# Kernel tuning notes

Measured on AMD Instinct MI355X. Metric: run time of the kernel, lower is better.

The kernel has to match this reference:

```python
import jax, jax.numpy as jnp
import numpy as np

# Dims: B=2, T=4 -> BT=8 frames; S=H*W=256 tokens/frame; L=25 stacked LLM layers; D=4096 llm hidden
BT, S, L, D = 8, 256, 25, 4096
C, NH = 1024, 8          # teacher_hid_size (hard-coded), num_heads
HD = C // NH             # 128
LAYER_IDX = np.array([24, 20, 16, 12, 8, 4, 0])  # num_layer=24 - arange(0,25,4)
J = len(LAYER_IDX)       # 7 distillation layers
SCALE = C ** -0.5        # NOTE: teacher_hid_size**-0.5, NOT head_dim**-0.5 (faithful to source)
EPS_LN, EPS_COS = 1e-5, 1e-8


def setup_inputs() -> dict:
    key = jax.random.key(0)
    ks = jax.random.split(key, 7)
    def n(k, shape, s=1.0):
        return jax.random.normal(k, shape, dtype=jnp.float32) * s
    return {
        "all_features": n(ks[0], (BT, S, L, D)),
        "teacher_features": n(ks[1], (BT, S, C)),
        "ln_gamma": jnp.ones((J, D), jnp.float32),
        "ln_beta": jnp.zeros((J, D), jnp.float32),
        "norm_w": n(ks[2], (J, C, D), 0.02),   # per-layer Linear(llm->teacher), no bias
        "input_w": n(ks[3], (C, D), 0.02),
        "input_b": n(ks[4], (C,), 0.02),
        "output_w": n(ks[5], (C, C), 0.02),
        "output_b": n(ks[6], (C,), 0.02),
    }


def reference(all_features, teacher_features, ln_gamma, ln_beta, norm_w,
              input_w, input_b, output_w, output_b):
    # Gather the distilled layers: [BT, S, J, D]
    x = all_features[:, :, LAYER_IDX]
    # Per-layer LayerNorm (each norm_layer[j] has its own affine params)
    mu = x.mean(-1, keepdims=True)
    var = ((x - mu) ** 2).mean(-1, keepdims=True)
    xn = (x - mu) * jax.lax.rsqrt(var + EPS_LN) * ln_gamma + ln_beta
    # Per-layer Linear (bias=False): stack -> vision_outputs [BT, S, J, C]
    vo = jnp.einsum('bsjd,jcd->bsjc', xn, norm_w)
    # input_layer on last hidden state: vision_input [BT, S, C]
    vin = jnp.einsum('bsd,cd->bsc', all_features[:, :, -1], input_w) + input_b
    # Hand-rolled multiplicative cross-attention over the J layer axis
    voh = vo.reshape(BT, S, J, NH, HD)
    q = voh[:, :, 0]        # [BT, S, NH, HD]
    kv = voh[:, :, 1:]      # [BT, S, J-1, NH, HD]
    scores = jnp.einsum('bshd,bskhd->bshk', q * SCALE, kv)   # [BT, S, NH, J-1]
    attn = jax.nn.softmax(scores, axis=-1)
    fuse = jnp.einsum('bshk,bskhd->bshd', attn, kv).reshape(BT, S, C)
    vf = vin + jnp.einsum('bsc,oc->bso', fuse, output_w) + output_b  # vision_feature
    # Cosine distillation loss vs teacher (torch CosineSimilarity eps=1e-8)
    na = jnp.maximum(jnp.linalg.norm(vf, axis=-1), EPS_COS)
    nb = jnp.maximum(jnp.linalg.norm(teacher_features, axis=-1), EPS_COS)
    cos = (vf * teacher_features).sum(-1) / (na * nb)        # [BT, S]
    # sum_i (1 - mean_s cos_i) / count_image, count_image = BT  ->  1 - mean over all
    return 1.0 - cos.mean()
```

## Files before the change

### kernel.cpp

```cpp
#include <hip/hip_runtime.h>
#include <cstdint>
#include <cstring>

#define M_TOK 2048
#define DDIM 4096
#define CDIM 1024
#define LTOT 25

typedef __bf16 bf16_t;
typedef __attribute__((ext_vector_type(8))) __bf16 bf16x8;
typedef __attribute__((ext_vector_type(4))) float f32x4;
typedef __attribute__((ext_vector_type(16))) float f32x16;
typedef __attribute__((ext_vector_type(8))) int i32x8;
typedef __attribute__((ext_vector_type(4))) unsigned int u32x4;
typedef unsigned char u8;

__device__ __forceinline__ void gload16(const void* g, void* l) {
  __builtin_amdgcn_global_load_lds(
      (const __attribute__((address_space(1))) unsigned int*)g,
      (__attribute__((address_space(3))) unsigned int*)l, 16, 0, 0);
}

__device__ __forceinline__ unsigned int pk4_fp8(float x, float y, float z, float w) {
  int r = __builtin_amdgcn_cvt_pk_fp8_f32(x, y, 0, false);
  r = __builtin_amdgcn_cvt_pk_fp8_f32(z, w, r, true);
  return (unsigned int)r;
}

__global__ void cvt_fp8(const float* __restrict__ src, u8* __restrict__ dst, long n) {
  long stride = (long)gridDim.x * blockDim.x;
  for (long i = (long)blockIdx.x * blockDim.x + threadIdx.x; i * 8 < n; i += stride) {
    const float4* s4 = (const float4*)(src + i * 8);
    float4 a = s4[0], b = s4[1];
    uint2 pk;
    pk.x = pk4_fp8(a.x, a.y, a.z, a.w);
    pk.y = pk4_fp8(b.x, b.y, b.z, b.w);
    *(uint2*)(dst + i * 8) = pk;
  }
}

__global__ void cvt_bf16(const float* __restrict__ src, bf16_t* __restrict__ dst, long n) {
  long stride = (long)gridDim.x * blockDim.x;
  for (long i = (long)blockIdx.x * blockDim.x + threadIdx.x; i * 8 < n; i += stride) {
    const float4* s4 = (const float4*)(src + i * 8);
    float4 a = s4[0], b = s4[1];
    bf16_t o[8] = {(bf16_t)a.x, (bf16_t)a.y, (bf16_t)a.z, (bf16_t)a.w,
                   (bf16_t)b.x, (bf16_t)b.y, (bf16_t)b.z, (bf16_t)b.w};
    uint4 pk;
    __builtin_memcpy(&pk, o, 16);
    *(uint4*)(dst + i * 8) = pk;
  }
}

__global__ __launch_bounds__(256)
void ln_convert(const float* __restrict__ af, const float* __restrict__ gamma,
                const float* __restrict__ beta, u8* __restrict__ xn,
                int jBase, int fuse7)
{
  int m = blockIdx.x;
  int jl = blockIdx.y;
  int j = jBase + jl;
  int layer = (j < 7) ? (24 - 4 * j) : 24;
  const float4* row4 = (const float4*)(af + ((size_t)m * LTOT + layer) * DDIM);
  int tid = threadIdx.x;
  float4 v[4];
  float s = 0.f, ss = 0.f;
#pragma unroll
  for (int i = 0; i < 4; ++i) {
    v[i] = row4[i * 256 + tid];
    s += v[i].x + v[i].y + v[i].z + v[i].w;
    ss += v[i].x * v[i].x + v[i].y * v[i].y + v[i].z * v[i].z + v[i].w * v[i].w;
  }
  int lane = tid & 63, wv = tid >> 6;
#pragma unroll
  for (int off = 32; off; off >>= 1) { s += __shfl_xor(s, off); ss += __shfl_xor(ss, off); }
  __shared__ float red[8];
  if (lane == 0) { red[wv] = s; red[4 + wv] = ss; }
  __syncthreads();
  s = red[0] + red[1] + red[2] + red[3];
  ss = red[4] + red[5] + red[6] + red[7];
  float mu = 0.f, rs = 1.f;
  if (j < 7) {
    mu = s * (1.f / DDIM);
    float var = ss * (1.f / DDIM) - mu * mu;
    rs = rsqrtf(var + 1e-5f);
  }
  if (fuse7 && jl == 0) {
    u8* o7 = xn + ((size_t)7 * M_TOK + m) * DDIM;
#pragma unroll
    for (int i = 0; i < 4; ++i)
      ((unsigned int*)o7)[i * 256 + tid] = pk4_fp8(v[i].x, v[i].y, v[i].z, v[i].w);
  }
  u8* orow = xn + ((size_t)jl * M_TOK + m) * DDIM;
  int jw = (j < 7) ? j : 0;
  const float4* g4 = (const float4*)(gamma + (size_t)jw * DDIM);
  const float4* b4 = (const float4*)(beta + (size_t)jw * DDIM);
#pragma unroll
  for (int i = 0; i < 4; ++i) {
    float4 x = v[i];
    float4 ov;
    if (j < 7) {
      float4 g = g4[i * 256 + tid], bb = b4[i * 256 + tid];
      ov.x = (x.x - mu) * rs * g.x + bb.x;
      ov.y = (x.y - mu) * rs * g.y + bb.y;
      ov.z = (x.z - mu) * rs * g.z + bb.z;
      ov.w = (x.w - mu) * rs * g.w + bb.w;
    } else ov = x;
    ((unsigned int*)orow)[i * 256 + tid] = pk4_fp8(ov.x, ov.y, ov.z, ov.w);
  }
}

__global__ __launch_bounds__(256)
void prep(const float* __restrict__ af, const float* __restrict__ gamma,
          const float* __restrict__ beta, u8* __restrict__ xn,
          const float* __restrict__ norm_w, const float* __restrict__ input_w,
          const float* __restrict__ output_w, u8* __restrict__ wb8,
          bf16_t* __restrict__ owb)
{
  int tid = threadIdx.x;
  if (blockIdx.y == 7) {
    const long NW7 = (long)7 * CDIM * DDIM;
    const long NWI = (long)8 * CDIM * DDIM;
    const long TOT = NWI + (long)CDIM * CDIM;
    long stride = (long)gridDim.x * blockDim.x;
    for (long i = (long)blockIdx.x * blockDim.x + tid; i * 8 < TOT; i += stride) {
      long e = i * 8;
      const float* sp;
      if (e < NW7)      sp = norm_w + e;
      else if (e < NWI) sp = input_w + (e - NW7);
      else              sp = output_w + (e - NWI);
      const float4* s4 = (const float4*)sp;
      float4 a = s4[0], b = s4[1];
      if (e < NWI) {
        uint2 pk;
        pk.x = pk4_fp8(a.x, a.y, a.z, a.w);
        pk.y = pk4_fp8(b.x, b.y, b.z, b.w);
        *(uint2*)(wb8 + e) = pk;
      } else {
        bf16_t o[8] = {(bf16_t)a.x, (bf16_t)a.y, (bf16_t)a.z, (bf16_t)a.w,
                       (bf16_t)b.x, (bf16_t)b.y, (bf16_t)b.z, (bf16_t)b.w};
        uint4 pk;
        __builtin_memcpy(&pk, o, 16);
        *(uint4*)(owb + (e - NWI)) = pk;
      }
    }
    return;
  }
  int m = blockIdx.x;
  int jl = blockIdx.y;
  int layer = 24 - 4 * jl;
  const float4* row4 = (const float4*)(af + ((size_t)m * LTOT + layer) * DDIM);
  float4 v[4];
  float s = 0.f, ss = 0.f;
#pragma unroll
  for (int i = 0; i < 4; ++i) {
    v[i] = row4[i * 256 + tid];
    s += v[i].x + v[i].y + v[i].z + v[i].w;
    ss += v[i].x * v[i].x + v[i].y * v[i].y + v[i].z * v[i].z + v[i].w * v[i].w;
  }
  int lane = tid & 63, wv = tid >> 6;
#pragma unroll
  for (int off = 32; off; off >>= 1) { s += __shfl_xor(s, off); ss += __shfl_xor(ss, off); }
  __shared__ float red[8];
  if (lane == 0) { red[wv] = s; red[4 + wv] = ss; }
  __syncthreads();
  s = red[0] + red[1] + red[2] + red[3];
  ss = red[4] + red[5] + red[6] + red[7];
  float mu = s * (1.f / DDIM);
  float var = ss * (1.f / DDIM) - mu * mu;
  float rs = rsqrtf(var + 1e-5f);
  if (jl == 0) {
    u8* o7 = xn + ((size_t)7 * M_TOK + m) * DDIM;
#pragma unroll
    for (int i = 0; i < 4; ++i)
      ((unsigned int*)o7)[i * 256 + tid] = pk4_fp8(v[i].x, v[i].y, v[i].z, v[i].w);
  }
  u8* orow = xn + ((size_t)jl * M_TOK + m) * DDIM;
  const float4* g4 = (const float4*)(gamma + (size_t)jl * DDIM);
  const float4* b4 = (const float4*)(beta + (size_t)jl * DDIM);
#pragma unroll
  for (int i = 0; i < 4; ++i) {
    float4 x = v[i];
    float4 g = g4[i * 256 + tid], bb = b4[i * 256 + tid];
    float4 ov;
    ov.x = (x.x - mu) * rs * g.x + bb.x;
    ov.y = (x.y - mu) * rs * g.y + bb.y;
    ov.z = (x.z - mu) * rs * g.z + bb.z;
    ov.w = (x.w - mu) * rs * g.w + bb.w;
    ((unsigned int*)orow)[i * 256 + tid] = pk4_fp8(ov.x, ov.y, ov.z, ov.w);
  }
}

__global__ __launch_bounds__(512, 2)
void gemm256mx(const u8* __restrict__ A, const u8* __restrict__ B,
               bf16_t* __restrict__ Cout, const float* __restrict__ bias,
               int Mm, int Nn, int Kk, int jBase, int tilesPerJ, int tilesN)
{
  __shared__ __align__(16) u8 smem[131072];
  int nb = gridDim.x;
  int bid = blockIdx.x;
  if ((nb & 7) == 0) { int cpx = nb >> 3; bid = (bid & 7) * cpx + (bid >> 3); }
  int jl = bid / tilesPerJ;
  int t0 = bid % tilesPerJ;
  int bm = t0 / tilesN, bn = t0 % tilesN;
  int jg = jBase + jl;

  const u8* Aj = A + (size_t)jl * Mm * Kk + (size_t)bm * 256 * Kk;
  const u8* Bj = B + (size_t)jl * Nn * Kk + (size_t)bn * 256 * Kk;

  int tid = threadIdx.x;
  int lane = tid & 63, wid = tid >> 6;
  int wm = wid >> 2, wn = wid & 3;

  {
  }
  int S = wid * 64 + lane;
  int ib_s = S >> 7;
  int s2 = S & 127;
  int lh_s = s2 >> 6;
  int s3 = s2 & 63;
  int l31_s = s3 >> 1;
  int hs = s3 & 1;
  int h_s = hs ^ ((l31_s >> 2) & 1);
  int row_s = ib_s * 32 + l31_s;
  int koff_s = lh_s * 32 + h_s * 16;
  const u8* AsrcC0 = Aj + (size_t)row_s * Kk + koff_s;
  const u8* AsrcC1 = Aj + (size_t)(128 + row_s) * Kk + koff_s;
  const u8* BsrcC0 = Bj + (size_t)row_s * Kk + koff_s;
  const u8* BsrcC1 = Bj + (size_t)(128 + row_s) * Kk + koff_s;

  int l31 = lane & 31;
  int lh = lane >> 5;
  int x16 = ((l31 >> 2) & 1) << 4;
  int loOff = lh * 1024 + l31 * 32 + x16;
  int hiOff = lh * 1024 + l31 * 32 + (16 ^ x16);
  int bBlk = (wn >> 1) * 8192 + ((wn & 1) * 2) * 2048;

  int NT = Kk >> 6;
  f32x16 acc[4][2] = {};

#define STAGE4(tt_)                                                              \
  { gload16(AsrcC0 + (size_t)(tt_) * 64, &smem[((tt_) & 3) * 16384 + wid * 1024]); \
    gload16(AsrcC1 + (size_t)(tt_) * 64, &smem[((tt_) & 3) * 16384 + 8192 + wid * 1024]); \
    gload16(BsrcC0 + (size_t)(tt_) * 64, &smem[65536 + ((tt_) & 3) * 16384 + wid * 1024]); \
    gload16(BsrcC1 + (size_t)(tt_) * 64, &smem[65536 + ((tt_) & 3) * 16384 + 8192 + wid * 1024]); }

#define BAR() asm volatile("s_barrier" ::: "memory")

  STAGE4(0);
  if (NT > 1) STAGE4(1);
  if (NT > 2) STAGE4(2);
  if (NT > 2)      asm volatile("s_waitcnt vmcnt(8)" ::: "memory");
  else if (NT > 1) asm volatile("s_waitcnt vmcnt(4)" ::: "memory");
  else             asm volatile("s_waitcnt vmcnt(0)" ::: "memory");
  BAR();

#pragma unroll 1
  for (int t = 0; t < NT; ++t) {
    const u8* Ab = &smem[(t & 3) * 16384 + wm * 8192];
    const u8* Bb = &smem[65536 + (t & 3) * 16384 + bBlk];
    i32x8 Afr[4], Bfr[2];
#pragma unroll
    for (int ib = 0; ib < 4; ++ib) {
      u32x4 lo = *(const u32x4*)(Ab + ib * 2048 + loOff);
      u32x4 hi = *(const u32x4*)(Ab + ib * 2048 + hiOff);
      Afr[ib][0] = lo[0]; Afr[ib][1] = lo[1]; Afr[ib][2] = lo[2]; Afr[ib][3] = lo[3];
      Afr[ib][4] = hi[0]; Afr[ib][5] = hi[1]; Afr[ib][6] = hi[2]; Afr[ib][7] = hi[3];
    }
#pragma unroll
    for (int jb = 0; jb < 2; ++jb) {
      u32x4 lo = *(const u32x4*)(Bb + jb * 2048 + loOff);
      u32x4 hi = *(const u32x4*)(Bb + jb * 2048 + hiOff);
      Bfr[jb][0] = lo[0]; Bfr[jb][1] = lo[1]; Bfr[jb][2] = lo[2]; Bfr[jb][3] = lo[3];
      Bfr[jb][4] = hi[0]; Bfr[jb][5] = hi[1]; Bfr[jb][6] = hi[2]; Bfr[jb][7] = hi[3];
    }
    if (t + 3 < NT) STAGE4(t + 3);
    __builtin_amdgcn_s_setprio(1);
#pragma unroll
    for (int ib = 0; ib < 4; ++ib)
#pragma unroll
      for (int jb = 0; jb < 2; ++jb)
        acc[ib][jb] = __builtin_amdgcn_mfma_scale_f32_32x32x64_f8f6f4(
            Afr[ib], Bfr[jb], acc[ib][jb], 0, 0, 0, 127, 0, 127);
    __builtin_amdgcn_s_setprio(0);
    if (t + 1 < NT) {
      asm volatile("s_waitcnt lgkmcnt(0)" ::: "memory");
      if (t + 3 < NT)      asm volatile("s_waitcnt vmcnt(8)" ::: "memory");
      else if (t + 2 < NT) asm volatile("s_waitcnt vmcnt(4)" ::: "memory");
      else                 asm volatile("s_waitcnt vmcnt(0)" ::: "memory");
      BAR();
    }
  }
#undef STAGE4
#undef BAR

  int col0 = bn * 256 + wn * 64 + l31;
  int row0 = bm * 256 + wm * 128 + lh * 4;
  bf16_t* Cj = Cout + (size_t)jg * Mm * Nn;
  float bv0 = (jg == 7) ? bias[col0] : 0.f;
  float bv1 = (jg == 7) ? bias[col0 + 32] : 0.f;
#pragma unroll
  for (int ib = 0; ib < 4; ++ib) {
#pragma unroll
    for (int jb = 0; jb < 2; ++jb) {
      float bv = jb ? bv1 : bv0;
      int gc = col0 + jb * 32;
#pragma unroll
      for (int reg = 0; reg < 16; ++reg) {
        int gr = row0 + ib * 32 + (reg & 3) + 8 * (reg >> 2);
        Cj[(size_t)gr * Nn + gc] = (bf16_t)(acc[ib][jb][reg] + bv);
      }
    }
  }
}

__global__ __launch_bounds__(256)
void gemm_bt_epi(const bf16_t* __restrict__ A, const bf16_t* __restrict__ B,
                 float* __restrict__ Cout, const float* __restrict__ bias,
                 const bf16_t* __restrict__ vin, int Mm, int Nn, int Kk, int tilesN)
{
  __shared__ bf16_t As[128 * 64];
  __shared__ bf16_t Bs[128 * 64];
  int bid = blockIdx.x;
  int bm = bid / tilesN, bn = bid % tilesN;
  const bf16_t* Aj = A + (size_t)bm * 128 * Kk;
  const bf16_t* Bj = B + (size_t)bn * 128 * Kk;

  int tid = threadIdx.x;
  int lane = tid & 63, wv = tid >> 6;
  int wm = wv >> 1, wn = wv & 1;

  f32x4 acc[4][4] = {};

  int srow = wv * 32 + (lane >> 3);
  int scol = (lane & 7) * 8;
  const bf16_t* Ag = Aj + (size_t)srow * Kk + scol;
  const bf16_t* Bg = Bj + (size_t)srow * Kk + scol;

  for (int kt = 0; kt < Kk; kt += 64) {
#pragma unroll
    for (int c = 0; c < 4; ++c) {
      gload16(Ag + kt + (size_t)(c * 8) * Kk, &As[(wv * 32 + c * 8) * 64]);
      gload16(Bg + kt + (size_t)(c * 8) * Kk, &Bs[(wv * 32 + c * 8) * 64]);
    }
    __syncthreads();
#pragma unroll
    for (int ks = 0; ks < 2; ++ks) {
      int ko = ks * 32 + (lane >> 4) * 8;
      bf16x8 af[4], bfr[4];
#pragma unroll
      for (int i = 0; i < 4; ++i) {
        af[i] = *(const bf16x8*)&As[(wm * 64 + i * 16 + (lane & 15)) * 64 + ko];
        bfr[i] = *(const bf16x8*)&Bs[(wn * 64 + i * 16 + (lane & 15)) * 64 + ko];
      }
#pragma unroll
      for (int i = 0; i < 4; ++i)
#pragma unroll
        for (int j2 = 0; j2 < 4; ++j2)
          acc[i][j2] = __builtin_amdgcn_mfma_f32_16x16x32_bf16(af[i], bfr[j2], acc[i][j2], 0, 0, 0);
    }
    __syncthreads();
  }

  int rowBase = bm * 128 + wm * 64 + (lane >> 4) * 4;
  int colBase = bn * 128 + wn * 64 + (lane & 15);
#pragma unroll
  for (int i = 0; i < 4; ++i) {
#pragma unroll
    for (int j2 = 0; j2 < 4; ++j2) {
      int gn = colBase + j2 * 16;
      float bv = bias[gn];
#pragma unroll
      for (int r = 0; r < 4; ++r) {
        int gm = rowBase + i * 16 + r;
        Cout[(size_t)gm * Nn + gn] = acc[i][j2][r] + bv + (float)vin[(size_t)gm * Nn + gn];
      }
    }
  }
}

__global__ __launch_bounds__(512)
void attn_fuse(const bf16_t* __restrict__ vo, bf16_t* __restrict__ fuse)
{
  int m = blockIdx.x;
  int h = threadIdx.x >> 6;
  int lane = threadIdx.x & 63;
  const size_t slab = (size_t)M_TOK * CDIM;
  const bf16_t* base = vo + (size_t)m * CDIM + h * 128;
  float q0 = (float)base[lane], q1 = (float)base[lane + 64];
  float kv0[6], kv1[6], sc[6];
#pragma unroll
  for (int k = 0; k < 6; ++k) {
    const bf16_t* kb = base + (size_t)(k + 1) * slab;
    kv0[k] = (float)kb[lane]; kv1[k] = (float)kb[lane + 64];
    sc[k] = q0 * kv0[k] + q1 * kv1[k];
  }
#pragma unroll
  for (int k = 0; k < 6; ++k) {
#pragma unroll
    for (int off = 32; off; off >>= 1) sc[k] += __shfl_xor(sc[k], off);
    sc[k] *= 0.03125f;
  }
  float mx = sc[0];
#pragma unroll
  for (int k = 1; k < 6; ++k) mx = fmaxf(mx, sc[k]);
  float e[6], se = 0.f;
#pragma unroll
  for (int k = 0; k < 6; ++k) { e[k] = expf(sc[k] - mx); se += e[k]; }
  float inv = 1.f / se;
  float f0 = 0.f, f1 = 0.f;
#pragma unroll
  for (int k = 0; k < 6; ++k) { float w = e[k] * inv; f0 += w * kv0[k]; f1 += w * kv1[k]; }
  bf16_t* o = fuse + (size_t)m * CDIM + h * 128;
  o[lane] = (bf16_t)f0;
  o[lane + 64] = (bf16_t)f1;
}

__global__ __launch_bounds__(256)
void cos_row(const float* __restrict__ vf, const float* __restrict__ teacher, float* __restrict__ cosv)
{
  int m = blockIdx.x;
  int tid = threadIdx.x;
  float4 a = ((const float4*)(vf + (size_t)m * CDIM))[tid];
  float4 b = ((const float4*)(teacher + (size_t)m * CDIM))[tid];
  float dot = a.x * b.x + a.y * b.y + a.z * b.z + a.w * b.w;
  float na = a.x * a.x + a.y * a.y + a.z * a.z + a.w * a.w;
  float nb = b.x * b.x + b.y * b.y + b.z * b.z + b.w * b.w;
  int lane = tid & 63, wv = tid >> 6;
#pragma unroll
  for (int off = 32; off; off >>= 1) {
    dot += __shfl_xor(dot, off); na += __shfl_xor(na, off); nb += __shfl_xor(nb, off);
  }
  __shared__ float red[12];
  if (lane == 0) { red[wv] = dot; red[4 + wv] = na; red[8 + wv] = nb; }
  __syncthreads();
  if (tid == 0) {
    float d = red[0] + red[1] + red[2] + red[3];
    float x = red[4] + red[5] + red[6] + red[7];
    float y = red[8] + red[9] + red[10] + red[11];
    float den = fmaxf(sqrtf(x), 1e-8f) * fmaxf(sqrtf(y), 1e-8f);
    cosv[m] = d / den;
  }
}

__global__ __launch_bounds__(256)
void final_reduce(const float* __restrict__ cosv, float* __restrict__ out)
{
  int tid = threadIdx.x;
  float s = 0.f;
  for (int i = tid; i < M_TOK; i += 256) s += cosv[i];
  int lane = tid & 63, wv = tid >> 6;
#pragma unroll
  for (int off = 32; off; off >>= 1) s += __shfl_xor(s, off);
  __shared__ float red[4];
  if (lane == 0) red[wv] = s;
  __syncthreads();
  if (tid == 0) out[0] = 1.f - (red[0] + red[1] + red[2] + red[3]) * (1.f / M_TOK);
}

extern "C" void kernel_launch(void* const* d_in, const int* in_sizes, int n_in,
                              void* d_out, int out_size, void* d_ws, size_t ws_size,
                              hipStream_t stream)
{
  (void)in_sizes; (void)n_in; (void)out_size;
  const float* all_features = (const float*)d_in[0];
  const float* teacher = (const float*)d_in[1];
  const float* ln_gamma = (const float*)d_in[2];
  const float* ln_beta = (const float*)d_in[3];
  const float* norm_w = (const float*)d_in[4];
  const float* input_w = (const float*)d_in[5];
  const float* input_b = (const float*)d_in[6];
  const float* output_w = (const float*)d_in[7];
  const float* output_b = (const float*)d_in[8];
  float* out = (float*)d_out;
  char* ws = (char*)d_ws;

  const size_t M = M_TOK, D = DDIM, C = CDIM;
  const size_t xnB = 8 * M * D;
  const size_t wbB = 8 * C * D;
  const size_t owbB = C * C * 2;
  const size_t voB = 8 * M * C * 2;
  const size_t fuseB = M * C * 2;
  const size_t vfB = M * C * 4;
  const size_t cosB = M * 4;
  const size_t fastTotal = xnB + wbB + owbB + voB + fuseB + vfB + cosB;

  if (ws_size >= fastTotal) {
    u8* xn = (u8*)ws;
    u8* wb = (u8*)(ws + xnB);
    bf16_t* owb = (bf16_t*)(ws + xnB + wbB);
    bf16_t* vo = (bf16_t*)(ws + xnB + wbB + owbB);
    bf16_t* fuse = (bf16_t*)(ws + xnB + wbB + owbB + voB);
    float* vf = (float*)(ws + xnB + wbB + owbB + voB + fuseB);
    float* cosv = (float*)(ws + xnB + wbB + owbB + voB + fuseB + vfB);

    dim3 gp((unsigned)M, 8);
    prep<<<gp, 256, 0, stream>>>(all_features, ln_gamma, ln_beta, xn,
                                 norm_w, input_w, output_w, wb, owb);
    gemm256mx<<<256, 512, 0, stream>>>(xn, wb, vo, input_b,
                                       (int)M, (int)C, (int)D, 0, 32, 4);
    attn_fuse<<<(unsigned)M, 512, 0, stream>>>(vo, fuse);
    gemm_bt_epi<<<128, 256, 0, stream>>>(fuse, owb, vf, output_b, vo + (size_t)7 * M * C,
                                         (int)M, (int)C, (int)C, 8);
    cos_row<<<(unsigned)M, 256, 0, stream>>>(vf, teacher, cosv);
    final_reduce<<<1, 256, 0, stream>>>(cosv, out);
  } else {
    const size_t xn1B = M * D;
    const size_t wb1B = C * D;
    u8* xn1 = (u8*)ws;
    u8* wb1 = (u8*)(ws + xn1B);
    bf16_t* owb = (bf16_t*)(ws + xn1B + wb1B);
    bf16_t* vo = (bf16_t*)(ws + xn1B + wb1B + owbB);
    bf16_t* fuse = (bf16_t*)(ws + xn1B + wb1B + owbB + voB);
    float* vf = (float*)(ws + xn1B + wb1B + owbB + voB + fuseB);
    float* cosv = (float*)(ws + xn1B + wb1B + owbB + voB + fuseB + vfB);

    cvt_bf16<<<512, 256, 0, stream>>>(output_w, owb, (long)(C * C));
    for (int j = 0; j < 8; ++j) {
      const float* wsrc = (j < 7) ? (norm_w + (size_t)j * C * D) : input_w;
      cvt_fp8<<<2048, 256, 0, stream>>>(wsrc, wb1, (long)(C * D));
      dim3 g1((unsigned)M, 1);
      ln_convert<<<g1, 256, 0, stream>>>(all_features, ln_gamma, ln_beta, xn1, j, 0);
      gemm256mx<<<32, 512, 0, stream>>>(xn1, wb1, vo, input_b,
                                        (int)M, (int)C, (int)D, j, 32, 4);
    }
    attn_fuse<<<(unsigned)M, 512, 0, stream>>>(vo, fuse);
    gemm_bt_epi<<<128, 256, 0, stream>>>(fuse, owb, vf, output_b, vo + (size_t)7 * M * C,
                                         (int)M, (int)C, (int)C, 8);
    cos_row<<<(unsigned)M, 256, 0, stream>>>(vf, teacher, cosv);
    final_reduce<<<1, 256, 0, stream>>>(cosv, out);
  }
}
```

Before: 209.6 us.

## Shrink FP8 GEMM tile to 256x128 with 4 waves and triple buffering

The main FP8 MFMA GEMM moves from a 256x256 tile with 8 waves and a 4-stage LDS ring to a 256x128 tile with 4 waves and a 3-stage ring. LDS per block drops from 128KB to 72KB, and the grid doubles to 512 blocks. The aim is better CU coverage and occupancy on a GEMM that had only 256 blocks. In exchange, the smaller N tile lowers per-block reuse of A, so more A traffic goes to L2, and the prefetch depth is shorter.

```diff
diff --git a/kernel.cpp b/kernel.cpp
--- a/kernel.cpp
+++ b/kernel.cpp
@@ -191,12 +191,12 @@
   }
 }
 
-__global__ __launch_bounds__(512, 2)
+__global__ __launch_bounds__(256, 2)
 void gemm256mx(const u8* __restrict__ A, const u8* __restrict__ B,
                bf16_t* __restrict__ Cout, const float* __restrict__ bias,
                int Mm, int Nn, int Kk, int jBase, int tilesPerJ, int tilesN)
 {
-  __shared__ __align__(16) u8 smem[131072];
+  __shared__ __align__(16) u8 smem[73728];
   int nb = gridDim.x;
   int bid = blockIdx.x;
   if ((nb & 7) == 0) { int cpx = nb >> 3; bid = (bid & 7) * cpx + (bid >> 3); }
@@ -206,59 +206,71 @@
   int jg = jBase + jl;
 
   const u8* Aj = A + (size_t)jl * Mm * Kk + (size_t)bm * 256 * Kk;
-  const u8* Bj = B + (size_t)jl * Nn * Kk + (size_t)bn * 256 * Kk;
+  const u8* Bj = B + (size_t)jl * Nn * Kk + (size_t)bn * 128 * Kk;
 
   int tid = threadIdx.x;
   int lane = tid & 63, wid = tid >> 6;
-  int wm = wid >> 2, wn = wid & 3;
-
-  {
-  }
-  int S = wid * 64 + lane;
-  int ib_s = S >> 7;
-  int s2 = S & 127;
-  int lh_s = s2 >> 6;
-  int s3 = s2 & 63;
-  int l31_s = s3 >> 1;
-  int hs = s3 & 1;
-  int h_s = hs ^ ((l31_s >> 2) & 1);
-  int row_s = ib_s * 32 + l31_s;
-  int koff_s = lh_s * 32 + h_s * 16;
-  const u8* AsrcC0 = Aj + (size_t)row_s * Kk + koff_s;
-  const u8* AsrcC1 = Aj + (size_t)(128 + row_s) * Kk + koff_s;
-  const u8* BsrcC0 = Bj + (size_t)row_s * Kk + koff_s;
-  const u8* BsrcC1 = Bj + (size_t)(128 + row_s) * Kk + koff_s;
+  int wm = wid >> 1, wn = wid & 1;
+
+  const u8* Asrc[4];
+#pragma unroll
+  for (int c = 0; c < 4; ++c) {
+    int SA = wid * 4 + c;
+    int chunk = SA >> 3;
+    int T = (SA & 7) * 64 + lane;
+    int ib = T >> 7;
+    int lh_ = (T >> 6) & 1;
+    int l31_ = (T & 63) >> 1;
+    int h_ = (T & 1) ^ ((l31_ >> 2) & 1);
+    int row = chunk * 128 + ib * 32 + l31_;
+    int koff = lh_ * 32 + h_ * 16;
+    Asrc[c] = Aj + (size_t)row * Kk + koff;
+  }
+  const u8* Bsrc[2];
+#pragma unroll
+  for (int c = 0; c < 2; ++c) {
+    int SB = wid * 2 + c;
+    int T = SB * 64 + lane;
+    int ib = T >> 7;
+    int lh_ = (T >> 6) & 1;
+    int l31_ = (T & 63) >> 1;
+    int h_ = (T & 1) ^ ((l31_ >> 2) & 1);
+    int row = ib * 32 + l31_;
+    int koff = lh_ * 32 + h_ * 16;
+    Bsrc[c] = Bj + (size_t)row * Kk + koff;
+  }
 
   int l31 = lane & 31;
   int lh = lane >> 5;
   int x16 = ((l31 >> 2) & 1) << 4;
   int loOff = lh * 1024 + l31 * 32 + x16;
   int hiOff = lh * 1024 + l31 * 32 + (16 ^ x16);
-  int bBlk = (wn >> 1) * 8192 + ((wn & 1) * 2) * 2048;
 
   int NT = Kk >> 6;
   f32x16 acc[4][2] = {};
 
-#define STAGE4(tt_)                                                              \
-  { gload16(AsrcC0 + (size_t)(tt_) * 64, &smem[((tt_) & 3) * 16384 + wid * 1024]); \
-    gload16(AsrcC1 + (size_t)(tt_) * 64, &smem[((tt_) & 3) * 16384 + 8192 + wid * 1024]); \
-    gload16(BsrcC0 + (size_t)(tt_) * 64, &smem[65536 + ((tt_) & 3) * 16384 + wid * 1024]); \
-    gload16(BsrcC1 + (size_t)(tt_) * 64, &smem[65536 + ((tt_) & 3) * 16384 + 8192 + wid * 1024]); }
+#define STAGE(tt_, buf_)                                                         \
+  { u8* base_ = &smem[(buf_) * 24576];                                           \
+    _Pragma("unroll")                                                            \
+    for (int c_ = 0; c_ < 4; ++c_)                                               \
+      gload16(Asrc[c_] + (size_t)(tt_) * 64, base_ + (wid * 4 + c_) * 1024);     \
+    _Pragma("unroll")                                                            \
+    for (int c_ = 0; c_ < 2; ++c_)                                               \
+      gload16(Bsrc[c_] + (size_t)(tt_) * 64, base_ + 16384 + (wid * 2 + c_) * 1024); }
 
 #define BAR() asm volatile("s_barrier" ::: "memory")
 
-  STAGE4(0);
-  if (NT > 1) STAGE4(1);
-  if (NT > 2) STAGE4(2);
-  if (NT > 2)      asm volatile("s_waitcnt vmcnt(8)" ::: "memory");
-  else if (NT > 1) asm volatile("s_waitcnt vmcnt(4)" ::: "memory");
-  else             asm volatile("s_waitcnt vmcnt(0)" ::: "memory");
+  STAGE(0, 0);
+  if (NT > 1) STAGE(1, 1);
+  if (NT > 1) asm volatile("s_waitcnt vmcnt(6)" ::: "memory");
+  else        asm volatile("s_waitcnt vmcnt(0)" ::: "memory");
   BAR();
 
+  int buf = 0, buf2 = 2;
 #pragma unroll 1
   for (int t = 0; t < NT; ++t) {
-    const u8* Ab = &smem[(t & 3) * 16384 + wm * 8192];
-    const u8* Bb = &smem[65536 + (t & 3) * 16384 + bBlk];
+    const u8* Ab = &smem[buf * 24576 + wm * 8192];
+    const u8* Bb = &smem[buf * 24576 + 16384 + (wn * 2) * 2048];
     i32x8 Afr[4], Bfr[2];
 #pragma unroll
     for (int ib = 0; ib < 4; ++ib) {
@@ -274,7 +286,7 @@
       Bfr[jb][0] = lo[0]; Bfr[jb][1] = lo[1]; Bfr[jb][2] = lo[2]; Bfr[jb][3] = lo[3];
       Bfr[jb][4] = hi[0]; Bfr[jb][5] = hi[1]; Bfr[jb][6] = hi[2]; Bfr[jb][7] = hi[3];
     }
-    if (t + 3 < NT) STAGE4(t + 3);
+    if (t + 2 < NT) STAGE(t + 2, buf2);
     __builtin_amdgcn_s_setprio(1);
 #pragma unroll
     for (int ib = 0; ib < 4; ++ib)
@@ -285,16 +297,17 @@
     __builtin_amdgcn_s_setprio(0);
     if (t + 1 < NT) {
       asm volatile("s_waitcnt lgkmcnt(0)" ::: "memory");
-      if (t + 3 < NT)      asm volatile("s_waitcnt vmcnt(8)" ::: "memory");
-      else if (t + 2 < NT) asm volatile("s_waitcnt vmcnt(4)" ::: "memory");
-      else                 asm volatile("s_waitcnt vmcnt(0)" ::: "memory");
+      if (t + 2 < NT) asm volatile("s_waitcnt vmcnt(6)" ::: "memory");
+      else            asm volatile("s_waitcnt vmcnt(0)" ::: "memory");
       BAR();
     }
-  }
-#undef STAGE4
+    buf = (buf == 2) ? 0 : buf + 1;
+    buf2 = (buf2 == 2) ? 0 : buf2 + 1;
+  }
+#undef STAGE
 #undef BAR
 
-  int col0 = bn * 256 + wn * 64 + l31;
+  int col0 = bn * 128 + wn * 64 + l31;
   int row0 = bm * 256 + wm * 128 + lh * 4;
   bf16_t* Cj = Cout + (size_t)jg * Mm * Nn;
   float bv0 = (jg == 7) ? bias[col0] : 0.f;
@@ -497,8 +510,8 @@
     dim3 gp((unsigned)M, 8);
     prep<<<gp, 256, 0, stream>>>(all_features, ln_gamma, ln_beta, xn,
                                  norm_w, input_w, output_w, wb, owb);
-    gemm256mx<<<256, 512, 0, stream>>>(xn, wb, vo, input_b,
-                                       (int)M, (int)C, (int)D, 0, 32, 4);
+    gemm256mx<<<512, 256, 0, stream>>>(xn, wb, vo, input_b,
+                                       (int)M, (int)C, (int)D, 0, 64, 8);
     attn_fuse<<<(unsigned)M, 512, 0, stream>>>(vo, fuse);
     gemm_bt_epi<<<128, 256, 0, stream>>>(fuse, owb, vf, output_b, vo + (size_t)7 * M * C,
                                          (int)M, (int)C, (int)C, 8);
@@ -521,8 +534,8 @@
       cvt_fp8<<<2048, 256, 0, stream>>>(wsrc, wb1, (long)(C * D));
       dim3 g1((unsigned)M, 1);
       ln_convert<<<g1, 256, 0, stream>>>(all_features, ln_gamma, ln_beta, xn1, j, 0);
-      gemm256mx<<<32, 512, 0, stream>>>(xn1, wb1, vo, input_b,
-                                        (int)M, (int)C, (int)D, j, 32, 4);
+      gemm256mx<<<64, 256, 0, stream>>>(xn1, wb1, vo, input_b,
+                                        (int)M, (int)C, (int)D, j, 64, 8);
     }
     attn_fuse<<<(unsigned)M, 512, 0, stream>>>(vo, fuse);
     gemm_bt_epi<<<128, 256, 0, stream>>>(fuse, owb, vf, output_b, vo + (size_t)7 * M * C,
```

Measured after the change: 216.5 us. 1.03x slower.

## Process two K-tiles per barrier in the FP8 GEMM main loop

Applied to the files above, without the earlier changes.

The GEMM main loop now handles two 64-wide K tiles per iteration instead of one. At the start of each iteration it issues loads for the next two tiles, then computes the current pair, then fully drains outstanding loads and hits a single barrier. This halves the number of barriers and LDS waits. In exchange, prefetch depth is shorter and the drain is a blunt vmcnt(0), which may expose more global-load latency. The loop also assumes an even tile count.

```diff
diff --git a/kernel.cpp b/kernel.cpp
--- a/kernel.cpp
+++ b/kernel.cpp
@@ -212,8 +212,6 @@
   int lane = tid & 63, wid = tid >> 6;
   int wm = wid >> 2, wn = wid & 3;
 
-  {
-  }
   int S = wid * 64 + lane;
   int ib_s = S >> 7;
   int s2 = S & 127;
@@ -245,53 +243,54 @@
     gload16(BsrcC0 + (size_t)(tt_) * 64, &smem[65536 + ((tt_) & 3) * 16384 + wid * 1024]); \
     gload16(BsrcC1 + (size_t)(tt_) * 64, &smem[65536 + ((tt_) & 3) * 16384 + 8192 + wid * 1024]); }
 
+#define COMPUTE(tt_)                                                             \
+  { const u8* Ab_ = &smem[((tt_) & 3) * 16384 + wm * 8192];                      \
+    const u8* Bb_ = &smem[65536 + ((tt_) & 3) * 16384 + bBlk];                   \
+    i32x8 Afr[4], Bfr[2];                                                        \
+    _Pragma("unroll")                                                            \
+    for (int ib = 0; ib < 4; ++ib) {                                             \
+      u32x4 lo = *(const u32x4*)(Ab_ + ib * 2048 + loOff);                       \
+      u32x4 hi = *(const u32x4*)(Ab_ + ib * 2048 + hiOff);                       \
+      Afr[ib][0] = lo[0]; Afr[ib][1] = lo[1]; Afr[ib][2] = lo[2]; Afr[ib][3] = lo[3]; \
+      Afr[ib][4] = hi[0]; Afr[ib][5] = hi[1]; Afr[ib][6] = hi[2]; Afr[ib][7] = hi[3]; \
+    }                                                                            \
+    _Pragma("unroll")                                                            \
+    for (int jb = 0; jb < 2; ++jb) {                                             \
+      u32x4 lo = *(const u32x4*)(Bb_ + jb * 2048 + loOff);                       \
+      u32x4 hi = *(const u32x4*)(Bb_ + jb * 2048 + hiOff);                       \
+      Bfr[jb][0] = lo[0]; Bfr[jb][1] = lo[1]; Bfr[jb][2] = lo[2]; Bfr[jb][3] = lo[3]; \
+      Bfr[jb][4] = hi[0]; Bfr[jb][5] = hi[1]; Bfr[jb][6] = hi[2]; Bfr[jb][7] = hi[3]; \
+    }                                                                            \
+    __builtin_amdgcn_s_setprio(1);                                               \
+    _Pragma("unroll")                                                            \
+    for (int ib = 0; ib < 4; ++ib)                                               \
+      _Pragma("unroll")                                                          \
+      for (int jb = 0; jb < 2; ++jb)                                             \
+        acc[ib][jb] = __builtin_amdgcn_mfma_scale_f32_32x32x64_f8f6f4(           \
+            Afr[ib], Bfr[jb], acc[ib][jb], 0, 0, 0, 127, 0, 127);                \
+    __builtin_amdgcn_s_setprio(0); }
+
 #define BAR() asm volatile("s_barrier" ::: "memory")
 
   STAGE4(0);
   if (NT > 1) STAGE4(1);
-  if (NT > 2) STAGE4(2);
-  if (NT > 2)      asm volatile("s_waitcnt vmcnt(8)" ::: "memory");
-  else if (NT > 1) asm volatile("s_waitcnt vmcnt(4)" ::: "memory");
-  else             asm volatile("s_waitcnt vmcnt(0)" ::: "memory");
+  asm volatile("s_waitcnt vmcnt(0)" ::: "memory");
   BAR();
 
 #pragma unroll 1
-  for (int t = 0; t < NT; ++t) {
-    const u8* Ab = &smem[(t & 3) * 16384 + wm * 8192];
-    const u8* Bb = &smem[65536 + (t & 3) * 16384 + bBlk];
-    i32x8 Afr[4], Bfr[2];
-#pragma unroll
-    for (int ib = 0; ib < 4; ++ib) {
-      u32x4 lo = *(const u32x4*)(Ab + ib * 2048 + loOff);
-      u32x4 hi = *(const u32x4*)(Ab + ib * 2048 + hiOff);
-      Afr[ib][0] = lo[0]; Afr[ib][1] = lo[1]; Afr[ib][2] = lo[2]; Afr[ib][3] = lo[3];
-      Afr[ib][4] = hi[0]; Afr[ib][5] = hi[1]; Afr[ib][6] = hi[2]; Afr[ib][7] = hi[3];
-    }
-#pragma unroll
-    for (int jb = 0; jb < 2; ++jb) {
-      u32x4 lo = *(const u32x4*)(Bb + jb * 2048 + loOff);
-      u32x4 hi = *(const u32x4*)(Bb + jb * 2048 + hiOff);
-      Bfr[jb][0] = lo[0]; Bfr[jb][1] = lo[1]; Bfr[jb][2] = lo[2]; Bfr[jb][3] = lo[3];
-      Bfr[jb][4] = hi[0]; Bfr[jb][5] = hi[1]; Bfr[jb][6] = hi[2]; Bfr[jb][7] = hi[3];
-    }
+  for (int t = 0; t < NT; t += 2) {
+    if (t + 2 < NT) STAGE4(t + 2);
     if (t + 3 < NT) STAGE4(t + 3);
-    __builtin_amdgcn_s_setprio(1);
-#pragma unroll
-    for (int ib = 0; ib < 4; ++ib)
-#pragma unroll
-      for (int jb = 0; jb < 2; ++jb)
-        acc[ib][jb] = __builtin_amdgcn_mfma_scale_f32_32x32x64_f8f6f4(
-            Afr[ib], Bfr[jb], acc[ib][jb], 0, 0, 0, 127, 0, 127);
-    __builtin_amdgcn_s_setprio(0);
-    if (t + 1 < NT) {
+    COMPUTE(t);
+    COMPUTE(t + 1);
+    if (t + 2 < NT) {
       asm volatile("s_waitcnt lgkmcnt(0)" ::: "memory");
-      if (t + 3 < NT)      asm volatile("s_waitcnt vmcnt(8)" ::: "memory");
-      else if (t + 2 < NT) asm volatile("s_waitcnt vmcnt(4)" ::: "memory");
-      else                 asm volatile("s_waitcnt vmcnt(0)" ::: "memory");
+      asm volatile("s_waitcnt vmcnt(0)" ::: "memory");
       BAR();
     }
   }
 #undef STAGE4
+#undef COMPUTE
 #undef BAR
 
   int col0 = bn * 256 + wn * 64 + l31;
```

Result: slower. 215.2 us (+2.7%).
